# Kernel tuning notes

Hardware: AMD Instinct MI355X
Metric: run time of the kernel (lower is better)

## Reference

```python
import jax, jax.numpy as jnp
import numpy as np
from jax import lax

B, T, D_IN, D_OUT = 8, 4096, 256, 256


def setup_inputs() -> dict:
    key = jax.random.key(0)
    k1, k2, k3, k4, k5 = jax.random.split(key, 5)
    bound_in = 1.0 / np.sqrt(D_IN)
    return {
        "inputs": jax.random.normal(k1, (B, T, D_IN), dtype=jnp.float32),
        "mask": jnp.zeros((B, T, 1), dtype=jnp.float32),
        "W_in": jax.random.uniform(k2, (D_OUT, D_IN), jnp.float32, -bound_in, bound_in),
        "b_in": jax.random.uniform(k3, (D_OUT,), jnp.float32, -bound_in, bound_in),
        "W_f": jax.random.uniform(k4, (D_OUT, D_IN), jnp.float32, -bound_in, bound_in),
        "b_f": jax.random.uniform(k5, (D_OUT,), jnp.float32, -bound_in, bound_in),
    }


def _forget_mult(f, x):
    # h_t = f_t * x_t + (1 - f_t) * h_{t-1}, h_{-1} = 0 (torchqrnn ForgetMult, hidden_init=None)
    fT = jnp.swapaxes(f, 0, 1)  # (T, B, D)
    xT = jnp.swapaxes(x, 0, 1)

    def step(h, fx):
        ft, xt = fx
        h = ft * xt + (1.0 - ft) * h
        return h, h

    h0 = jnp.zeros(xT.shape[1:], dtype=x.dtype)  # (B, D)
    _, hs = lax.scan(step, h0, (fT, xT))
    return jnp.swapaxes(hs, 0, 1)  # (B, T, D)


def reference(inputs, mask, W_in, b_in, W_f, b_f):
    # right_to_left = False -> no flips
    x = jnp.tanh(jnp.einsum("btd,od->bto", inputs, W_in) + b_in)
    f = jax.nn.sigmoid(jnp.einsum("btd,od->bto", inputs, W_f) + b_f + mask * 10000.0)
    return _forget_mult(f, x)
```

## Files before the change

### kernel.cpp

```cpp
#include <hip/hip_runtime.h>
#include <math.h>


typedef _Float16 f16x8 __attribute__((ext_vector_type(8)));
typedef float f32x4 __attribute__((ext_vector_type(4)));
typedef float f32x16 __attribute__((ext_vector_type(16)));

constexpr int B_ = 8, T_ = 4096, D_ = 256, K_ = 256;
constexpr int M_ = B_ * T_;
constexpr int CHUNK = 64;
constexpr int NCH = T_ / CHUNK;

struct alignas(4) XF { _Float16 x, f; };

__device__ __forceinline__ float fexp2(float a) { return __builtin_amdgcn_exp2f(a); }
__device__ __forceinline__ float frcp(float a) { return __builtin_amdgcn_rcpf(a); }
constexpr float L2E = 1.4426950408889634f;

__device__ __forceinline__ float fast_sigmoid(float z) {
  return frcp(1.f + fexp2(-z * L2E));
}
__device__ __forceinline__ float fast_tanh(float z) {
  const float t = fexp2(-2.f * L2E * fabsf(z));
  return copysignf((1.f - t) * frcp(1.f + t), z);
}

__global__ __launch_bounds__(256) void wconv(const float* __restrict__ Win,
                                             const float* __restrict__ Wf,
                                             _Float16* __restrict__ Wh2) {
  const int t = blockIdx.x * 256 + threadIdx.x;
  const int n = t & 255;
  const int kc = (t >> 8) & 3;
  const int mat = (t >> 10) & 1;
  const int kk = t >> 11;
  const float* s = (mat ? Wf : Win) + (size_t)n * K_ + kk * 32 + kc * 8;
  f32x4 a = *(const f32x4*)s;
  f32x4 b = *(const f32x4*)(s + 4);
  f16x8 o;
  o[0] = (_Float16)a[0]; o[1] = (_Float16)a[1];
  o[2] = (_Float16)a[2]; o[3] = (_Float16)a[3];
  o[4] = (_Float16)b[0]; o[5] = (_Float16)b[1];
  o[6] = (_Float16)b[2]; o[7] = (_Float16)b[3];
  *(f16x8*)(Wh2 + (size_t)t * 8) = o;
}

__global__ __launch_bounds__(256) void gemm_fused(
    const float* __restrict__ A, const _Float16* __restrict__ Wh2,
    const float* __restrict__ bin, const float* __restrict__ bfv,
    const float* __restrict__ mask, XF* __restrict__ xf,
    float* __restrict__ Ap, float* __restrict__ Hp) {
  __shared__ __align__(16) char smem[65536];
  char* ldsA = smem;
  char* ldsW = smem + 4096;

  const int tid = threadIdx.x;
  const int w = tid >> 6, lane = tid & 63;
  const int mw = w >> 1, nw = w & 1;
  const int nl = lane & 31, kh = lane >> 5;
  const int ml = mw * 32 + nl;
  const int row0b = blockIdx.x * 64;

  f32x16 acc[2][4];
#pragma unroll
  for (int mat = 0; mat < 2; ++mat)
#pragma unroll
    for (int nt = 0; nt < 4; ++nt) acc[mat][nt] = (f32x16)(0.f);

  const int am = tid >> 2, apc = tid & 3, akc = (apc - am) & 3;
  const float* agp = A + (size_t)(row0b + am) * K_ + akc * 8;
  char* const alds = ldsA + tid * 16;

  for (int kk = 0; kk < 8; ++kk) {
    {
      const float* p = agp + kk * 32;
      f32x4 lo = *(const f32x4*)p;
      f32x4 hi = *(const f32x4*)(p + 4);
      f16x8 t;
      t[0] = (_Float16)lo[0]; t[1] = (_Float16)lo[1];
      t[2] = (_Float16)lo[2]; t[3] = (_Float16)lo[3];
      t[4] = (_Float16)hi[0]; t[5] = (_Float16)hi[1];
      t[6] = (_Float16)hi[2]; t[7] = (_Float16)hi[3];
      *(f16x8*)alds = t;
    }
#pragma unroll
    for (int j = 0; j < 8; ++j) {
      const int c = j * 256 + tid;
      f16x8 v = *(const f16x8*)(Wh2 + (size_t)kk * 16384 + (size_t)c * 8);
      *(f16x8*)(ldsW + (size_t)c * 16) = v;
    }
    __syncthreads();

    f16x8 afr[2];
#pragma unroll
    for (int i2 = 0; i2 < 2; ++i2) {
      const int kc = i2 * 2 + kh;
      const int pc = (kc + ml) & 3;
      afr[i2] = *(const f16x8*)(ldsA + (ml * 4 + pc) * 16);
    }
#pragma unroll
    for (int mat = 0; mat < 2; ++mat)
#pragma unroll
      for (int nt = 0; nt < 4; ++nt) {
        const int n = nw * 128 + nt * 32 + nl;
#pragma unroll
        for (int i2 = 0; i2 < 2; ++i2) {
          const int kc = i2 * 2 + kh;
          f16x8 bfr = *(const f16x8*)(ldsW + ((mat * 4 + kc) * 256 + n) * 16);
          acc[mat][nt] = __builtin_amdgcn_mfma_f32_32x32x16_f16(
              afr[i2], bfr, acc[mat][nt], 0, 0, 0);
        }
      }
    __syncthreads();
  }

  float bx[4], bf[4];
#pragma unroll
  for (int nt = 0; nt < 4; ++nt) {
    const int col = nw * 128 + nt * 32 + nl;
    bx[nt] = bin[col];
    bf[nt] = bfv[col];
  }
  float madd[16];
  int rowl[16];
#pragma unroll
  for (int reg = 0; reg < 16; ++reg) {
    const int rl = mw * 32 + (reg & 3) + 8 * (reg >> 2) + 4 * kh;
    rowl[reg] = rl;
    madd[reg] = 10000.f * mask[row0b + rl];
  }
#pragma unroll
  for (int nt = 0; nt < 4; ++nt) {
    const int col = nw * 128 + nt * 32 + nl;
#pragma unroll
    for (int reg = 0; reg < 16; ++reg) {
      const float zx = acc[0][nt][reg] + bx[nt];
      const float zf = acc[1][nt][reg] + bf[nt] + madd[reg];
      XF v;
      v.x = (_Float16)fast_tanh(zx);
      v.f = (_Float16)fast_sigmoid(zf);
      *(XF*)(smem + ((size_t)rowl[reg] * D_ + col) * 4) = v;
      xf[((size_t)row0b + rowl[reg]) * D_ + col] = v;
    }
  }
  __syncthreads();

  const int d = tid;
  float Aa = 1.f, h = 0.f;
#pragma unroll 8
  for (int t = 0; t < CHUNK; ++t) {
    const XF v = *(const XF*)(smem + ((size_t)t * D_ + d) * 4);
    const float f = (float)v.f;
    const float a = 1.f - f;
    h = f * (float)v.x + a * h;
    Aa *= a;
  }
  Ap[(size_t)blockIdx.x * D_ + d] = Aa;
  Hp[(size_t)blockIdx.x * D_ + d] = h;
}

__global__ __launch_bounds__(256) void scan_final(const XF* __restrict__ xf,
                                                  const float* __restrict__ Ap,
                                                  const float* __restrict__ Hp,
                                                  float* __restrict__ out) {
  const int g = blockIdx.x;
  const int b = g >> 6, c = g & 63;
  const int d = threadIdx.x;
  const float* ap = Ap + ((size_t)b * NCH) * D_ + d;
  const float* hp = Hp + ((size_t)b * NCH) * D_ + d;
  float h = 0.f;
  for (int j = 0; j < c; ++j) h = hp[(size_t)j * D_] + ap[(size_t)j * D_] * h;

  const size_t base = (size_t)g * CHUNK * D_ + d;
#pragma unroll 8
  for (int t = 0; t < CHUNK; ++t) {
    const XF v = xf[base + (size_t)t * D_];
    const float f = (float)v.f;
    h = f * (float)v.x + (1.f - f) * h;
    out[base + (size_t)t * D_] = h;
  }
}

extern "C" void kernel_launch(void* const* d_in, const int* in_sizes, int n_in,
                              void* d_out, int out_size, void* d_ws, size_t ws_size,
                              hipStream_t stream) {
  const float* inputs = (const float*)d_in[0];
  const float* mask   = (const float*)d_in[1];
  const float* W_in   = (const float*)d_in[2];
  const float* b_in   = (const float*)d_in[3];
  const float* W_f    = (const float*)d_in[4];
  const float* b_f    = (const float*)d_in[5];
  float* out = (float*)d_out;
  char* ws = (char*)d_ws;

  constexpr size_t XFSZ = (size_t)M_ * D_ * sizeof(XF);
  constexpr size_t WSZ  = (size_t)2 * 256 * 256 * 2;
  constexpr size_t SUM  = (size_t)B_ * NCH * D_ * sizeof(float);

  XF* xf = (XF*)ws;
  _Float16* Wh2 = (_Float16*)(ws + XFSZ);
  float* Ap = (float*)(ws + XFSZ + WSZ);
  float* Hp = Ap + SUM / sizeof(float);

  wconv<<<64, 256, 0, stream>>>(W_in, W_f, Wh2);
  gemm_fused<<<512, 256, 0, stream>>>(inputs, Wh2, b_in, b_f, mask, xf, Ap, Hp);
  scan_final<<<512, 256, 0, stream>>>(xf, Ap, Hp, out);
}
```

Baseline: 141.3 us.

## Preload full A tile into swizzled LDS and register-prefetch weight slices

The GEMM kernel now loads and converts the block's whole 64x256 input tile into LDS once, with an XOR swizzle, instead of one K-slice per iteration. The next weight K-slice is prefetched into registers while the current slice's MFMAs run, so global loads overlap compute. A launch-bounds hint of two blocks per CU is added. The cost is more register pressure from the eight prefetched vectors, and the full 64KB of LDS per block is now used during the GEMM phase, which could limit residency.

```diff
diff --git a/kernel.cpp b/kernel.cpp
--- a/kernel.cpp
+++ b/kernel.cpp
@@ -44,21 +44,22 @@
   *(f16x8*)(Wh2 + (size_t)t * 8) = o;
 }
 
-__global__ __launch_bounds__(256) void gemm_fused(
+__global__ __launch_bounds__(256, 2) void gemm_fused(
     const float* __restrict__ A, const _Float16* __restrict__ Wh2,
     const float* __restrict__ bin, const float* __restrict__ bfv,
     const float* __restrict__ mask, XF* __restrict__ xf,
     float* __restrict__ Ap, float* __restrict__ Hp) {
   __shared__ __align__(16) char smem[65536];
   char* ldsA = smem;
-  char* ldsW = smem + 4096;
+  char* ldsW = smem + 32768;
 
   const int tid = threadIdx.x;
   const int w = tid >> 6, lane = tid & 63;
   const int mw = w >> 1, nw = w & 1;
   const int nl = lane & 31, kh = lane >> 5;
   const int ml = mw * 32 + nl;
-  const int row0b = blockIdx.x * 64;
+  const int g = blockIdx.x;
+  const int row0b = g * CHUNK;
 
   f32x16 acc[2][4];
 #pragma unroll
@@ -66,36 +67,45 @@
 #pragma unroll
     for (int nt = 0; nt < 4; ++nt) acc[mat][nt] = (f32x16)(0.f);
 
-  const int am = tid >> 2, apc = tid & 3, akc = (apc - am) & 3;
-  const float* agp = A + (size_t)(row0b + am) * K_ + akc * 8;
-  char* const alds = ldsA + tid * 16;
-
-  for (int kk = 0; kk < 8; ++kk) {
-    {
-      const float* p = agp + kk * 32;
-      f32x4 lo = *(const f32x4*)p;
-      f32x4 hi = *(const f32x4*)(p + 4);
+  {
+    const int am = tid >> 2;
+    const int ak4 = (tid & 3) * 8;
+    const float* agp = A + (size_t)(row0b + am) * K_ + ak4 * 8;
+#pragma unroll
+    for (int j = 0; j < 8; ++j) {
+      const int kcg = ak4 + j;
+      f32x4 lo = *(const f32x4*)(agp + j * 8);
+      f32x4 hi = *(const f32x4*)(agp + j * 8 + 4);
       f16x8 t;
       t[0] = (_Float16)lo[0]; t[1] = (_Float16)lo[1];
       t[2] = (_Float16)lo[2]; t[3] = (_Float16)lo[3];
       t[4] = (_Float16)hi[0]; t[5] = (_Float16)hi[1];
       t[6] = (_Float16)hi[2]; t[7] = (_Float16)hi[3];
-      *(f16x8*)alds = t;
-    }
-#pragma unroll
-    for (int j = 0; j < 8; ++j) {
-      const int c = j * 256 + tid;
-      f16x8 v = *(const f16x8*)(Wh2 + (size_t)kk * 16384 + (size_t)c * 8);
-      *(f16x8*)(ldsW + (size_t)c * 16) = v;
-    }
+      *(f16x8*)(ldsA + am * 512 + ((kcg ^ (am & 31)) << 4)) = t;
+    }
+  }
+
+  f16x8 wreg[8];
+#pragma unroll
+  for (int j = 0; j < 8; ++j)
+    wreg[j] = *(const f16x8*)(Wh2 + (size_t)(j * 256 + tid) * 8);
+
+  for (int kk = 0; kk < 8; ++kk) {
+#pragma unroll
+    for (int j = 0; j < 8; ++j)
+      *(f16x8*)(ldsW + (size_t)(j * 256 + tid) * 16) = wreg[j];
     __syncthreads();
-
+    if (kk < 7) {
+#pragma unroll
+      for (int j = 0; j < 8; ++j)
+        wreg[j] = *(const f16x8*)(Wh2 + (size_t)(kk + 1) * 16384 +
+                                  (size_t)(j * 256 + tid) * 8);
+    }
     f16x8 afr[2];
 #pragma unroll
     for (int i2 = 0; i2 < 2; ++i2) {
-      const int kc = i2 * 2 + kh;
-      const int pc = (kc + ml) & 3;
-      afr[i2] = *(const f16x8*)(ldsA + (ml * 4 + pc) * 16);
+      const int kcg = kk * 4 + i2 * 2 + kh;
+      afr[i2] = *(const f16x8*)(ldsA + ml * 512 + ((kcg ^ (ml & 31)) << 4));
     }
 #pragma unroll
     for (int mat = 0; mat < 2; ++mat)
@@ -105,7 +115,7 @@
 #pragma unroll
         for (int i2 = 0; i2 < 2; ++i2) {
           const int kc = i2 * 2 + kh;
-          f16x8 bfr = *(const f16x8*)(ldsW + ((mat * 4 + kc) * 256 + n) * 16);
+          f16x8 bfr = *(const f16x8*)(ldsW + (size_t)((mat * 4 + kc) * 256 + n) * 16);
           acc[mat][nt] = __builtin_amdgcn_mfma_f32_32x32x16_f16(
               afr[i2], bfr, acc[mat][nt], 0, 0, 0);
         }
@@ -154,8 +164,8 @@
     h = f * (float)v.x + a * h;
     Aa *= a;
   }
-  Ap[(size_t)blockIdx.x * D_ + d] = Aa;
-  Hp[(size_t)blockIdx.x * D_ + d] = h;
+  Ap[(size_t)g * D_ + d] = Aa;
+  Hp[(size_t)g * D_ + d] = h;
 }
 
 __global__ __launch_bounds__(256) void scan_final(const XF* __restrict__ xf,
@@ -194,7 +204,7 @@
 
   constexpr size_t XFSZ = (size_t)M_ * D_ * sizeof(XF);
   constexpr size_t WSZ  = (size_t)2 * 256 * 256 * 2;
-  constexpr size_t SUM  = (size_t)B_ * NCH * D_ * sizeof(float);
+  constexpr size_t SUM  = (size_t)M_ / CHUNK * D_ * sizeof(float);
 
   XF* xf = (XF*)ws;
   _Float16* Wh2 = (_Float16*)(ws + XFSZ);
```

After: 129.9 us. 8.1% less time.
